# Performance work log

Hardware: AMD Instinct MI355X
Metric: run time of the kernel (lower is better)

The kernel has to match this reference:

```python
import jax, jax.numpy as jnp
import numpy as np

N, T, INPUT_DIM, HIDDEN_DIM = 8, 4096, 128, 128


def setup_inputs() -> dict:
    key = jax.random.key(0)
    k_h, k_wq, k_bq, k_wk, k_bk = jax.random.split(key, 5)
    s = 1.0 / np.sqrt(INPUT_DIM)
    return {
        "H": jax.random.normal(k_h, (N, T, INPUT_DIM), dtype=jnp.float32),
        "Wq": jax.random.uniform(k_wq, (INPUT_DIM, HIDDEN_DIM), jnp.float32, -s, s),
        "bq": jax.random.uniform(k_bq, (HIDDEN_DIM,), jnp.float32, -s, s),
        "Wk": jax.random.uniform(k_wk, (INPUT_DIM, HIDDEN_DIM), jnp.float32, -s, s),
        "bk": jax.random.uniform(k_bk, (HIDDEN_DIM,), jnp.float32, -s, s),
    }


def reference(H, Wq, bq, Wk, bk):
    # Q, K: [N, T, hidden]
    Q = jnp.einsum("ntd,dh->nth", H, Wq) + bq
    K = jnp.einsum("ntd,dh->nth", H, Wk) + bk
    # Faithful quirk: original scales by sqrt(K.transpose(-1,-2).size(-1)) == sqrt(T),
    # NOT sqrt(hidden_dim).
    T_ = H.shape[1]
    scale = 1.0 / jnp.sqrt(jnp.asarray(T_, dtype=H.dtype))
    A = jnp.einsum("nth,nsh->nts", Q, K) * scale  # [N, T, T]
    A = jax.nn.softmax(A, axis=-1)
    # Attention applied directly to H (no V projection), plus residual.
    return jnp.einsum("nts,nsd->ntd", A, H) + H
```

## Files before the change

kernel.cpp:

```cpp
#include <hip/hip_runtime.h>
#include <hip/hip_bf16.h>

typedef __attribute__((ext_vector_type(4))) float f32x4;
typedef __attribute__((ext_vector_type(16))) float f32x16;
typedef __attribute__((ext_vector_type(8))) short s16x8;
typedef unsigned int u32;

#define DEVINL static __device__ __forceinline__

constexpr int TDIM = 4096;
constexpr int DDIM = 128;
constexpr float QSCALE = 1.4426950408889634f / 64.0f;

DEVINL unsigned short f2bf(float f) {
  union { float f; unsigned u; } v; v.f = f;
  unsigned r = v.u + 0x7fffu + ((v.u >> 16) & 1u);
  return (unsigned short)(r >> 16);
}

__global__ __launch_bounds__(256) void prep_kernel(
    const float* __restrict__ Wq, const float* __restrict__ Wk,
    const float* __restrict__ bq, unsigned short* __restrict__ Mt,
    float* __restrict__ u) {
  int idx = blockIdx.x * 256 + threadIdx.x;
  int e = idx >> 7, d = idx & 127;
  float acc = 0.f;
#pragma unroll 4
  for (int h = 0; h < 128; ++h) acc += Wq[d * 128 + h] * Wk[e * 128 + h];
  Mt[e * 128 + d] = f2bf(acc);
  if (blockIdx.x == 0 && threadIdx.x < 128) {
    float a = 0.f;
#pragma unroll 4
    for (int h = 0; h < 128; ++h) a += Wk[threadIdx.x * 128 + h] * bq[h];
    u[threadIdx.x] = a;
  }
}

__global__ __launch_bounds__(256) void proj_kernel(
    const float* __restrict__ H, const unsigned short* __restrict__ Mt,
    const float* __restrict__ u, char* __restrict__ Qb,
    char* __restrict__ Kb, char* __restrict__ Vt) {
  __shared__ __align__(16) unsigned short hs[64][136];
  __shared__ __align__(16) char qs[16384];
  __shared__ __align__(16) char kt[16384];
  __shared__ __align__(16) char vt[16384];
  int b = blockIdx.x;
  int n = b >> 6;
  int t0 = (b & 63) << 6;
  int tid = threadIdx.x;
  const float* Hrow = H + (size_t)(n * TDIM + t0) * DDIM;
#pragma unroll
  for (int k = 0; k < 8; ++k) {
    int e = tid + k * 256;
    int r = e >> 5;
    int c = (e & 31) << 2;
    f32x4 v = *(const f32x4*)(Hrow + r * DDIM + c);
    unsigned short bf[4] = {f2bf(v.x), f2bf(v.y), f2bf(v.z), f2bf(v.w)};
    unsigned short* p = &hs[r][c];
    p[0] = bf[0]; p[1] = bf[1]; p[2] = bf[2]; p[3] = bf[3];
    int kbyte = r * 256 + ((c * 2) ^ ((r & 15) << 4));
    unsigned short* kp = (unsigned short*)(kt + kbyte);
    kp[0] = bf[0]; kp[1] = bf[1]; kp[2] = bf[2]; kp[3] = bf[3];
    int p32 = r >> 5, tl = r & 31;
#pragma unroll
    for (int j = 0; j < 4; ++j) {
      int d = c + j;
      int rq = d >> 2;
      int byte = p32 * 8192 + rq * 256 +
                 (((d & 3) * 64 + tl * 2) ^ ((rq & 15) << 4));
      *(unsigned short*)(vt + byte) = bf[j];
    }
  }
  __syncthreads();
  int w = tid >> 6, ln = tid & 63;
  int lm = ln & 15, lg = ln >> 4;
  int m0 = w * 16;
  s16x8 af[4];
#pragma unroll
  for (int kf = 0; kf < 4; ++kf)
    af[kf] = *(const s16x8*)&hs[m0 + lm][kf * 32 + lg * 8];
#pragma unroll
  for (int nt = 0; nt < 8; ++nt) {
    f32x4 acc = {0.f, 0.f, 0.f, 0.f};
#pragma unroll
    for (int kf = 0; kf < 4; ++kf) {
      s16x8 bfr = *(const s16x8*)&Mt[(nt * 16 + lm) * 128 + kf * 32 + lg * 8];
      acc = __builtin_amdgcn_mfma_f32_16x16x32_bf16(af[kf], bfr, acc, 0, 0, 0);
    }
    int e = nt * 16 + lm;
    float bv = u[e];
#pragma unroll
    for (int i = 0; i < 4; ++i) {
      int tl = m0 + lg * 4 + i;
      int byte = tl * 256 + ((e * 2) ^ ((tl & 15) << 4));
      *(unsigned short*)(qs + byte) = f2bf((acc[i] + bv) * QSCALE);
    }
  }
  __syncthreads();
  size_t base = (size_t)(n * TDIM + t0) * 256;
  size_t vbase = (size_t)(n * 128 + (t0 >> 5)) * 8192;
#pragma unroll
  for (int k = 0; k < 4; ++k) {
    int off = tid * 16 + k * 4096;
    *(f32x4*)(Qb + base + off) = *(const f32x4*)(qs + off);
    *(f32x4*)(Kb + base + off) = *(const f32x4*)(kt + off);
    *(f32x4*)(Vt + vbase + off) = *(const f32x4*)(vt + off);
  }
}

DEVINL void stage8(const char* g, char* s, int ln) {
#pragma unroll
  for (int j = 0; j < 8; ++j) {
    __builtin_amdgcn_global_load_lds(
        (const __attribute__((address_space(1))) void*)(g + j * 1024 + ln * 16),
        (__attribute__((address_space(3))) void*)(s + j * 1024), 16, 0, 0);
  }
}

__global__ __launch_bounds__(128, 2) void attn_kernel(
    const char* __restrict__ Qsw, const char* __restrict__ Ksw,
    const char* __restrict__ Vsw, u32* __restrict__ OutU,
    u32* __restrict__ OpU, float* __restrict__ Lp) {
  __shared__ __align__(16) char kbuf[2][8192];
  __shared__ __align__(16) char vbuf[2][8192];
  int b = blockIdx.x;
  int n = b & 7;
  int st = (b >> 3) & 3;
  int q0 = (b >> 5) << 7;
  int tid = threadIdx.x;
  int w = tid >> 6, ln = tid & 63;
  int q32 = ln & 31, hi = ln >> 5;
  int qrow = q0 + w * 64;
  int swz = (q32 & 15) << 4;

  const char* Kn = Ksw + (size_t)n * (TDIM * 256);
  const char* Vn = Vsw + (size_t)n * (128 * 8192);
  int kv0 = st * 1024;

  const char* Qlo = Qsw + (size_t)(n * TDIM + qrow + q32) * 256;
  const char* Qhi = Qlo + 32 * 256;
  s16x8 qfl[8], qfh[8];
#pragma unroll
  for (int d = 0; d < 8; ++d) {
    int off = (d * 32 + hi * 16) ^ swz;
    qfl[d] = *(const s16x8*)(Qlo + off);
    qfh[d] = *(const s16x8*)(Qhi + off);
  }

  f32x16 o[8];
#pragma unroll
  for (int i = 0; i < 8; ++i) o[i] = (f32x16)0.0f;
  float lsl = 0.f, lsh = 0.f;

  {
    const char* g = w ? (Vn + (size_t)(kv0 >> 5) * 8192)
                      : (Kn + (size_t)kv0 * 256);
    stage8(g, w ? vbuf[0] : kbuf[0], ln);
  }
  __syncthreads();

  for (int it = 0; it < 32; ++it) {
    int c = it & 1;
    if (it < 31) {
      int kvn = kv0 + (it + 1) * 32;
      const char* g = w ? (Vn + (size_t)(kvn >> 5) * 8192)
                        : (Kn + (size_t)kvn * 256);
      stage8(g, w ? vbuf[c ^ 1] : kbuf[c ^ 1], ln);
    }
    const char* kb = kbuf[c];
    const char* vb = vbuf[c];

    f32x16 sl = (f32x16)0.0f, sh = (f32x16)0.0f;
    __builtin_amdgcn_s_setprio(1);
#pragma unroll
    for (int d = 0; d < 8; ++d) {
      s16x8 ka = *(const s16x8*)(kb + (q32 * 256 + ((d * 32 + hi * 16) ^ swz)));
      sl = __builtin_amdgcn_mfma_f32_32x32x16_bf16(ka, qfl[d], sl, 0, 0, 0);
      sh = __builtin_amdgcn_mfma_f32_32x32x16_bf16(ka, qfh[d], sh, 0, 0, 0);
    }
    __builtin_amdgcn_s_setprio(0);

#pragma unroll
    for (int r = 0; r < 16; ++r) {
      sl[r] = __builtin_amdgcn_exp2f(sl[r]);
      lsl += sl[r];
      sh[r] = __builtin_amdgcn_exp2f(sh[r]);
      lsh += sh[r];
    }

    s16x8 pal[2], pah[2];
    {
      u32 P2[8];
#pragma unroll
      for (int r = 0; r < 8; ++r)
        asm("v_cvt_pk_bf16_f32 %0, %1, %2"
            : "=v"(P2[r]) : "v"(sl[2 * r]), "v"(sl[2 * r + 1]));
#pragma unroll
      for (int b2 = 0; b2 < 2; ++b2) {
        u32 a0 = P2[b2 * 4 + 0], c0 = P2[b2 * 4 + 2];
        u32 a1 = P2[b2 * 4 + 1], c1 = P2[b2 * 4 + 3];
        asm("v_permlane32_swap_b32 %0, %1" : "+v"(a0), "+v"(c0));
        asm("v_permlane32_swap_b32 %0, %1" : "+v"(a1), "+v"(c1));
        union { u32 u[4]; s16x8 v; } pk;
        pk.u[0] = a0; pk.u[1] = a1; pk.u[2] = c0; pk.u[3] = c1;
        pal[b2] = pk.v;
      }
#pragma unroll
      for (int r = 0; r < 8; ++r)
        asm("v_cvt_pk_bf16_f32 %0, %1, %2"
            : "=v"(P2[r]) : "v"(sh[2 * r]), "v"(sh[2 * r + 1]));
#pragma unroll
      for (int b2 = 0; b2 < 2; ++b2) {
        u32 a0 = P2[b2 * 4 + 0], c0 = P2[b2 * 4 + 2];
        u32 a1 = P2[b2 * 4 + 1], c1 = P2[b2 * 4 + 3];
        asm("v_permlane32_swap_b32 %0, %1" : "+v"(a0), "+v"(c0));
        asm("v_permlane32_swap_b32 %0, %1" : "+v"(a1), "+v"(c1));
        union { u32 u[4]; s16x8 v; } pk;
        pk.u[0] = a0; pk.u[1] = a1; pk.u[2] = c0; pk.u[3] = c1;
        pah[b2] = pk.v;
      }
    }

    __builtin_amdgcn_s_setprio(1);
#pragma unroll
    for (int ks = 0; ks < 2; ++ks) {
#pragma unroll
      for (int dt = 0; dt < 4; ++dt) {
        int rq = dt * 8 + (q32 >> 2);
        s16x8 vv = *(const s16x8*)(vb + rq * 256 +
            (((q32 & 3) * 64 + ks * 32 + hi * 16) ^ ((rq & 15) << 4)));
        o[dt] = __builtin_amdgcn_mfma_f32_32x32x16_bf16(pal[ks], vv, o[dt], 0, 0, 0);
        o[4 + dt] = __builtin_amdgcn_mfma_f32_32x32x16_bf16(pah[ks], vv, o[4 + dt], 0, 0, 0);
      }
    }
    __builtin_amdgcn_s_setprio(0);
    __syncthreads();
  }

  u32* Ob = (st < 2 ? OutU : OpU) + (st & 1) * 64;
#pragma unroll
  for (int r = 0; r < 16; ++r) {
    int qr = (r & 3) + 8 * (r >> 2) + 4 * hi;
    size_t rl = (size_t)(n * TDIM + qrow + qr) * 128;
    size_t rh = rl + (size_t)32 * 128;
    u32 a, bb;
    asm("v_cvt_pk_bf16_f32 %0, %1, %2" : "=v"(a) : "v"(o[0][r]), "v"(o[1][r]));
    asm("v_cvt_pk_bf16_f32 %0, %1, %2" : "=v"(bb) : "v"(o[2][r]), "v"(o[3][r]));
    Ob[rl + q32] = a;
    Ob[rl + 32 + q32] = bb;
    asm("v_cvt_pk_bf16_f32 %0, %1, %2" : "=v"(a) : "v"(o[4][r]), "v"(o[5][r]));
    asm("v_cvt_pk_bf16_f32 %0, %1, %2" : "=v"(bb) : "v"(o[6][r]), "v"(o[7][r]));
    Ob[rh + q32] = a;
    Ob[rh + 32 + q32] = bb;
  }
  Lp[(size_t)(n * TDIM + qrow + q32) * 8 + st * 2 + hi] = lsl;
  Lp[(size_t)(n * TDIM + qrow + 32 + q32) * 8 + st * 2 + hi] = lsh;
}

__global__ __launch_bounds__(256) void merge_kernel(
    u32* __restrict__ OutU, const u32* __restrict__ OpU,
    const float* __restrict__ Lp, const float* __restrict__ H) {
  int gid = blockIdx.x * 256 + threadIdx.x;
  int row = gid >> 6;
  int pi = gid & 63;
  int q32 = pi & 31, k = pi >> 5;
  f32x4 la = *(const f32x4*)(Lp + (size_t)row * 8);
  f32x4 lb = *(const f32x4*)(Lp + (size_t)row * 8 + 4);
  float il = 1.0f / (la.x + la.y + la.z + la.w + lb.x + lb.y + lb.z + lb.w);
  size_t rb = (size_t)row * 128;
  u32 p0 = OutU[rb + pi], p1 = OutU[rb + 64 + pi];
  u32 p2 = OpU[rb + pi],  p3 = OpU[rb + 64 + pi];
#define BL(x) __builtin_bit_cast(float, (u32)((x) << 16))
#define BH(x) __builtin_bit_cast(float, (u32)((x) & 0xffff0000u))
  float slo = BL(p0) + BL(p1) + BL(p2) + BL(p3);
  float shi = BH(p0) + BH(p1) + BH(p2) + BH(p3);
#undef BL
#undef BH
  int d0 = k * 64 + q32, d1 = d0 + 32;
  float* Outf = (float*)OutU;
  Outf[rb + d0] = slo * il + H[rb + d0];
  Outf[rb + d1] = shi * il + H[rb + d1];
}

extern "C" void kernel_launch(void* const* d_in, const int* in_sizes, int n_in,
                              void* d_out, int out_size, void* d_ws, size_t ws_size,
                              hipStream_t stream) {
  const float* H  = (const float*)d_in[0];
  const float* Wq = (const float*)d_in[1];
  const float* bq = (const float*)d_in[2];
  const float* Wk = (const float*)d_in[3];
  const float* bk = (const float*)d_in[4];
  (void)bk;
  u32* OutU = (u32*)d_out;
  char* ws = (char*)d_ws;
  unsigned short* Mt = (unsigned short*)(ws);
  float* u = (float*)(ws + 32768);
  char* Qb = ws + 65536;
  char* Kb = Qb + 8388608;
  char* Vt = Kb + 8388608;
  u32* OpU = (u32*)(Vt + 8388608);
  float* Lp = (float*)(ws + 65536 + 3 * 8388608 + 16777216);

  prep_kernel<<<64, 256, 0, stream>>>(Wq, Wk, bq, Mt, u);
  proj_kernel<<<512, 256, 0, stream>>>(H, Mt, u, Qb, Kb, Vt);
  attn_kernel<<<1024, 128, 0, stream>>>(Qb, Kb, Vt, OutU, OpU, Lp);
  merge_kernel<<<8192, 256, 0, stream>>>(OutU, OpU, Lp, H);
}
```

Measured before the change: 113.7 us.

## Split attention block into four 32-row waves with shared K/V staging

Reorganizes the attention kernel from two waves of 64 query rows each into four waves of 32 rows each. All four waves cooperatively stage K and V halves into LDS. QK^T is split over the head dimension into two independent accumulators that are summed before exp. This halves per-wave accumulator registers to allow higher occupancy and more latency hiding, at the cost of less K/V fragment reuse per LDS read.

```diff
diff --git a/kernel.cpp b/kernel.cpp
--- a/kernel.cpp
+++ b/kernel.cpp
@@ -108,16 +108,16 @@
   }
 }
 
-DEVINL void stage8(const char* g, char* s, int ln) {
-#pragma unroll
-  for (int j = 0; j < 8; ++j) {
+DEVINL void stage4(const char* g, char* s, int ln) {
+#pragma unroll
+  for (int j = 0; j < 4; ++j) {
     __builtin_amdgcn_global_load_lds(
         (const __attribute__((address_space(1))) void*)(g + j * 1024 + ln * 16),
         (__attribute__((address_space(3))) void*)(s + j * 1024), 16, 0, 0);
   }
 }
 
-__global__ __launch_bounds__(128, 2) void attn_kernel(
+__global__ __launch_bounds__(256, 4) void attn_kernel(
     const char* __restrict__ Qsw, const char* __restrict__ Ksw,
     const char* __restrict__ Vsw, u32* __restrict__ OutU,
     u32* __restrict__ OpU, float* __restrict__ Lp) {
@@ -130,32 +130,30 @@
   int tid = threadIdx.x;
   int w = tid >> 6, ln = tid & 63;
   int q32 = ln & 31, hi = ln >> 5;
-  int qrow = q0 + w * 64;
+  int qrow = q0 + w * 32;
   int swz = (q32 & 15) << 4;
 
   const char* Kn = Ksw + (size_t)n * (TDIM * 256);
   const char* Vn = Vsw + (size_t)n * (128 * 8192);
   int kv0 = st * 1024;
 
-  const char* Qlo = Qsw + (size_t)(n * TDIM + qrow + q32) * 256;
-  const char* Qhi = Qlo + 32 * 256;
-  s16x8 qfl[8], qfh[8];
-#pragma unroll
-  for (int d = 0; d < 8; ++d) {
-    int off = (d * 32 + hi * 16) ^ swz;
-    qfl[d] = *(const s16x8*)(Qlo + off);
-    qfh[d] = *(const s16x8*)(Qhi + off);
-  }
-
-  f32x16 o[8];
-#pragma unroll
-  for (int i = 0; i < 8; ++i) o[i] = (f32x16)0.0f;
-  float lsl = 0.f, lsh = 0.f;
+  const char* Qn = Qsw + (size_t)(n * TDIM + qrow + q32) * 256;
+  s16x8 qf[8];
+#pragma unroll
+  for (int d = 0; d < 8; ++d)
+    qf[d] = *(const s16x8*)(Qn + ((d * 32 + hi * 16) ^ swz));
+
+  f32x16 o[4];
+#pragma unroll
+  for (int dt = 0; dt < 4; ++dt) o[dt] = (f32x16)0.0f;
+  float lsum = 0.f;
 
   {
-    const char* g = w ? (Vn + (size_t)(kv0 >> 5) * 8192)
-                      : (Kn + (size_t)kv0 * 256);
-    stage8(g, w ? vbuf[0] : kbuf[0], ln);
+    const char* g = (w < 2)
+        ? (Kn + (size_t)kv0 * 256 + w * 4096)
+        : (Vn + (size_t)(kv0 >> 5) * 8192 + (w - 2) * 4096);
+    char* dst = (w < 2) ? (kbuf[0] + w * 4096) : (vbuf[0] + (w - 2) * 4096);
+    stage4(g, dst, ln);
   }
   __syncthreads();
 
@@ -163,38 +161,43 @@
     int c = it & 1;
     if (it < 31) {
       int kvn = kv0 + (it + 1) * 32;
-      const char* g = w ? (Vn + (size_t)(kvn >> 5) * 8192)
-                        : (Kn + (size_t)kvn * 256);
-      stage8(g, w ? vbuf[c ^ 1] : kbuf[c ^ 1], ln);
+      const char* g = (w < 2)
+          ? (Kn + (size_t)kvn * 256 + w * 4096)
+          : (Vn + (size_t)(kvn >> 5) * 8192 + (w - 2) * 4096);
+      char* dst = (w < 2) ? (kbuf[c ^ 1] + w * 4096)
+                          : (vbuf[c ^ 1] + (w - 2) * 4096);
+      stage4(g, dst, ln);
     }
     const char* kb = kbuf[c];
     const char* vb = vbuf[c];
 
-    f32x16 sl = (f32x16)0.0f, sh = (f32x16)0.0f;
+    f32x16 sa = (f32x16)0.0f, sb = (f32x16)0.0f;
     __builtin_amdgcn_s_setprio(1);
 #pragma unroll
-    for (int d = 0; d < 8; ++d) {
-      s16x8 ka = *(const s16x8*)(kb + (q32 * 256 + ((d * 32 + hi * 16) ^ swz)));
-      sl = __builtin_amdgcn_mfma_f32_32x32x16_bf16(ka, qfl[d], sl, 0, 0, 0);
-      sh = __builtin_amdgcn_mfma_f32_32x32x16_bf16(ka, qfh[d], sh, 0, 0, 0);
+    for (int d = 0; d < 4; ++d) {
+      s16x8 ka0 = *(const s16x8*)(kb + (q32 * 256 + ((d * 32 + hi * 16) ^ swz)));
+      s16x8 ka1 = *(const s16x8*)(kb + (q32 * 256 + (((d + 4) * 32 + hi * 16) ^ swz)));
+      sa = __builtin_amdgcn_mfma_f32_32x32x16_bf16(ka0, qf[d], sa, 0, 0, 0);
+      sb = __builtin_amdgcn_mfma_f32_32x32x16_bf16(ka1, qf[d + 4], sb, 0, 0, 0);
     }
     __builtin_amdgcn_s_setprio(0);
 
+    f32x16 p0;
+    float ls = 0.f;
 #pragma unroll
     for (int r = 0; r < 16; ++r) {
-      sl[r] = __builtin_amdgcn_exp2f(sl[r]);
-      lsl += sl[r];
-      sh[r] = __builtin_amdgcn_exp2f(sh[r]);
-      lsh += sh[r];
-    }
-
-    s16x8 pal[2], pah[2];
+      p0[r] = __builtin_amdgcn_exp2f(sa[r] + sb[r]);
+      ls += p0[r];
+    }
+    lsum += ls;
+
+    s16x8 pa[2];
     {
       u32 P2[8];
 #pragma unroll
       for (int r = 0; r < 8; ++r)
         asm("v_cvt_pk_bf16_f32 %0, %1, %2"
-            : "=v"(P2[r]) : "v"(sl[2 * r]), "v"(sl[2 * r + 1]));
+            : "=v"(P2[r]) : "v"(p0[2 * r]), "v"(p0[2 * r + 1]));
 #pragma unroll
       for (int b2 = 0; b2 < 2; ++b2) {
         u32 a0 = P2[b2 * 4 + 0], c0 = P2[b2 * 4 + 2];
@@ -203,21 +206,7 @@
         asm("v_permlane32_swap_b32 %0, %1" : "+v"(a1), "+v"(c1));
         union { u32 u[4]; s16x8 v; } pk;
         pk.u[0] = a0; pk.u[1] = a1; pk.u[2] = c0; pk.u[3] = c1;
-        pal[b2] = pk.v;
-      }
-#pragma unroll
-      for (int r = 0; r < 8; ++r)
-        asm("v_cvt_pk_bf16_f32 %0, %1, %2"
-            : "=v"(P2[r]) : "v"(sh[2 * r]), "v"(sh[2 * r + 1]));
-#pragma unroll
-      for (int b2 = 0; b2 < 2; ++b2) {
-        u32 a0 = P2[b2 * 4 + 0], c0 = P2[b2 * 4 + 2];
-        u32 a1 = P2[b2 * 4 + 1], c1 = P2[b2 * 4 + 3];
-        asm("v_permlane32_swap_b32 %0, %1" : "+v"(a0), "+v"(c0));
-        asm("v_permlane32_swap_b32 %0, %1" : "+v"(a1), "+v"(c1));
-        union { u32 u[4]; s16x8 v; } pk;
-        pk.u[0] = a0; pk.u[1] = a1; pk.u[2] = c0; pk.u[3] = c1;
-        pah[b2] = pk.v;
+        pa[b2] = pk.v;
       }
     }
 
@@ -229,8 +218,7 @@
         int rq = dt * 8 + (q32 >> 2);
         s16x8 vv = *(const s16x8*)(vb + rq * 256 +
             (((q32 & 3) * 64 + ks * 32 + hi * 16) ^ ((rq & 15) << 4)));
-        o[dt] = __builtin_amdgcn_mfma_f32_32x32x16_bf16(pal[ks], vv, o[dt], 0, 0, 0);
-        o[4 + dt] = __builtin_amdgcn_mfma_f32_32x32x16_bf16(pah[ks], vv, o[4 + dt], 0, 0, 0);
+        o[dt] = __builtin_amdgcn_mfma_f32_32x32x16_bf16(pa[ks], vv, o[dt], 0, 0, 0);
       }
     }
     __builtin_amdgcn_s_setprio(0);
@@ -242,19 +230,13 @@
   for (int r = 0; r < 16; ++r) {
     int qr = (r & 3) + 8 * (r >> 2) + 4 * hi;
     size_t rl = (size_t)(n * TDIM + qrow + qr) * 128;
-    size_t rh = rl + (size_t)32 * 128;
     u32 a, bb;
     asm("v_cvt_pk_bf16_f32 %0, %1, %2" : "=v"(a) : "v"(o[0][r]), "v"(o[1][r]));
     asm("v_cvt_pk_bf16_f32 %0, %1, %2" : "=v"(bb) : "v"(o[2][r]), "v"(o[3][r]));
     Ob[rl + q32] = a;
     Ob[rl + 32 + q32] = bb;
-    asm("v_cvt_pk_bf16_f32 %0, %1, %2" : "=v"(a) : "v"(o[4][r]), "v"(o[5][r]));
-    asm("v_cvt_pk_bf16_f32 %0, %1, %2" : "=v"(bb) : "v"(o[6][r]), "v"(o[7][r]));
-    Ob[rh + q32] = a;
-    Ob[rh + 32 + q32] = bb;
-  }
-  Lp[(size_t)(n * TDIM + qrow + q32) * 8 + st * 2 + hi] = lsl;
-  Lp[(size_t)(n * TDIM + qrow + 32 + q32) * 8 + st * 2 + hi] = lsh;
+  }
+  Lp[(size_t)(n * TDIM + qrow + q32) * 8 + st * 2 + hi] = lsum;
 }
 
 __global__ __launch_bounds__(256) void merge_kernel(
@@ -303,6 +285,6 @@
 
   prep_kernel<<<64, 256, 0, stream>>>(Wq, Wk, bq, Mt, u);
   proj_kernel<<<512, 256, 0, stream>>>(H, Mt, u, Qb, Kb, Vt);
-  attn_kernel<<<1024, 128, 0, stream>>>(Qb, Kb, Vt, OutU, OpU, Lp);
+  attn_kernel<<<1024, 256, 0, stream>>>(Qb, Kb, Vt, OutU, OpU, Lp);
   merge_kernel<<<8192, 256, 0, stream>>>(OutU, OpU, Lp, H);
 }
```

After: 277.8 us. 2.44x slower.
